# Optimization experiments

Measured on AMD Instinct MI355X. Metric: run time of the kernel, lower is better.

The kernel has to match this reference:

```python
import jax, jax.numpy as jnp
import numpy as np

N, E, D, H, C, HID, ED = 50000, 800000, 128, 8, 16, 512, 32


def setup_inputs() -> dict:
    key = jax.random.key(0)
    ks = jax.random.split(key, 16)
    s = 0.05
    return {
        "h": jax.random.normal(ks[0], (N, D), jnp.float32),
        "edge_index": jax.random.randint(ks[1], (2, E), 0, N, jnp.int64),
        "edge_attr": jax.random.normal(ks[2], (E, ED), jnp.float32),
        "w1": jax.random.normal(ks[3], (D, HID), jnp.float32) * s,
        "b1": jnp.zeros((HID,), jnp.float32),
        "w2": jax.random.normal(ks[4], (HID, D), jnp.float32) * s,
        "b2": jnp.zeros((D,), jnp.float32),
        "ln_g": jnp.ones((D,), jnp.float32),
        "ln_b": jnp.zeros((D,), jnp.float32),
        "Wl": jax.random.normal(ks[5], (D, H * C), jnp.float32) * s,
        "bl": jnp.zeros((H * C,), jnp.float32),
        "Wr": jax.random.normal(ks[6], (D, H * C), jnp.float32) * s,
        "br": jnp.zeros((H * C,), jnp.float32),
        "We": jax.random.normal(ks[7], (ED, H * C), jnp.float32) * s,
        "att": jax.random.normal(ks[8], (H, C), jnp.float32) * s,
        "bias_out": jnp.zeros((H * C,), jnp.float32),
    }


def _layer_norm(x, g, b, eps=1e-5):
    mu = jnp.mean(x, axis=-1, keepdims=True)
    var = jnp.var(x, axis=-1, keepdims=True)
    return (x - mu) * jax.lax.rsqrt(var + eps) * g + b


def reference(h, edge_index, edge_attr, w1, b1, w2, b2, ln_g, ln_b,
              Wl, bl, Wr, br, We, att, bias_out):
    # FFN + residual + LayerNorm (dropout = identity in eval)
    u = jax.nn.relu(h @ w1 + b1) @ w2 + b2
    v = _layer_norm(h + u, ln_g, ln_b)

    src, dst = edge_index[0], edge_index[1]
    # GATv2Conv: separate source/target transforms + edge transform
    xl = (v @ Wl + bl).reshape(N, H, C)
    xr = (v @ Wr + br).reshape(N, H, C)
    xe = (edge_attr @ We).reshape(E, H, C)
    x = jax.nn.leaky_relu(xl[src] + xr[dst] + xe, 0.2)  # [E,H,C]
    logits = jnp.einsum("ehc,hc->eh", x, att)            # [E,H]
    # segment softmax over incoming edges of each destination node
    m = jax.lax.stop_gradient(jax.ops.segment_max(logits, dst, num_segments=N))
    ex = jnp.exp(logits - m[dst])
    den = jax.ops.segment_sum(ex, dst, num_segments=N)
    alpha = ex / den[dst]                                # [E,H]
    msg = xl[src] * alpha[..., None]                     # [E,H,C]
    w = jax.ops.segment_sum(msg, dst, num_segments=N).reshape(N, H * C) + bias_out
    output = _layer_norm(w + v, ln_g, ln_b)
    return output, alpha
```

## Files before the change

kernel.cpp:

```cpp
#include <hip/hip_runtime.h>
#include <math.h>

#define N_NODES 50000
#define E_EDGES 800000
#define D_DIM   128
#define H_HEADS 8
#define C_CH    16
#define HID_DIM 512
#define ED_DIM  32

typedef __attribute__((ext_vector_type(8))) short short8;
typedef __attribute__((ext_vector_type(4))) float f32x4;

__device__ __forceinline__ short f2bf(float f) {
    unsigned u = __float_as_uint(f);
    return (short)((u + 0x7FFFu + ((u >> 16) & 1u)) >> 16);
}
__device__ __forceinline__ float bf2f(short s) {
    return __uint_as_float(((unsigned)(unsigned short)s) << 16);
}

__global__ __launch_bounds__(64) void repack_kernel(
    const float* __restrict__ w1, const float* __restrict__ w2,
    const float* __restrict__ Wl, const float* __restrict__ Wr,
    const float* __restrict__ We,
    short8* __restrict__ w1p, short8* __restrict__ w2p,
    short8* __restrict__ Wlp, short8* __restrict__ Wrp,
    short8* __restrict__ Wep)
{
    int b = blockIdx.x;
    const float* src; short8* dst; int Nw, nc, rel;
    if (b < 128)      { src = w1; dst = w1p; Nw = 512; nc = 4;  rel = b; }
    else if (b < 256) { src = w2; dst = w2p; Nw = 128; nc = 16; rel = b - 128; }
    else if (b < 288) { src = Wl; dst = Wlp; Nw = 128; nc = 4;  rel = b - 256; }
    else if (b < 320) { src = Wr; dst = Wrp; Nw = 128; nc = 4;  rel = b - 288; }
    else              { src = We; dst = Wep; Nw = 128; nc = 1;  rel = b - 320; }
    int t = rel / nc, c = rel % nc;
    int l = threadIdx.x, quad = l >> 4, col = l & 15;
    short8 r;
    #pragma unroll
    for (int j = 0; j < 8; ++j)
        r[j] = f2bf(src[(size_t)(c * 32 + quad * 8 + j) * Nw + t * 16 + col]);
    dst[(size_t)rel * 64 + l] = r;
}

__global__ __launch_bounds__(256) void count_kernel(
    const int* __restrict__ edge_index, unsigned* __restrict__ cnt,
    unsigned short* __restrict__ rank)
{
    int e = blockIdx.x * 256 + threadIdx.x;
    int dst = edge_index[E_EDGES + e];
    rank[e] = (unsigned short)atomicAdd(&cnt[dst], 1u);
}

__global__ __launch_bounds__(256) void node_ffn_mfma(
    const float* __restrict__ h,
    const float* __restrict__ b1, const float* __restrict__ b2,
    const float* __restrict__ ln_g, const float* __restrict__ ln_b,
    const float* __restrict__ bl, const float* __restrict__ br,
    const short8* __restrict__ w1p, const short8* __restrict__ w2p,
    const short8* __restrict__ Wlp, const short8* __restrict__ Wrp,
    float* __restrict__ v_out,
    unsigned short* __restrict__ xl_bf_out, unsigned short* __restrict__ xr_bf_out)
{
    __shared__ short hid_bf[16 * 520];
    __shared__ float v_s[16 * 132];
    __shared__ short v_bf[16 * 136];

    const int tid = threadIdx.x;
    const int w = tid >> 6, lane = tid & 63;
    const int m = lane & 15, quad = lane >> 4;
    const int n0 = blockIdx.x * 16;

    short8 af[4];
    #pragma unroll
    for (int c = 0; c < 4; ++c) {
        const float* hp = h + (size_t)(n0 + m) * 128 + c * 32 + quad * 8;
        float4 p0 = ((const float4*)hp)[0];
        float4 p1 = ((const float4*)hp)[1];
        short8 a;
        a[0] = f2bf(p0.x); a[1] = f2bf(p0.y); a[2] = f2bf(p0.z); a[3] = f2bf(p0.w);
        a[4] = f2bf(p1.x); a[5] = f2bf(p1.y); a[6] = f2bf(p1.z); a[7] = f2bf(p1.w);
        af[c] = a;
    }

    {
        f32x4 acc[8];
        #pragma unroll
        for (int t = 0; t < 8; ++t) acc[t] = (f32x4){0.f, 0.f, 0.f, 0.f};
        #pragma unroll
        for (int t = 0; t < 8; ++t) {
            int tile = w * 8 + t;
            #pragma unroll
            for (int c = 0; c < 4; ++c) {
                short8 bf = w1p[(size_t)(tile * 4 + c) * 64 + lane];
                acc[t] = __builtin_amdgcn_mfma_f32_16x16x32_bf16(af[c], bf, acc[t], 0, 0, 0);
            }
        }
        #pragma unroll
        for (int t = 0; t < 8; ++t) {
            int col = (w * 8 + t) * 16 + m;
            float bias = b1[col];
            #pragma unroll
            for (int r = 0; r < 4; ++r) {
                int row = quad * 4 + r;
                hid_bf[row * 520 + col] = f2bf(fmaxf(acc[t][r] + bias, 0.f));
            }
        }
    }
    __syncthreads();

    {
        f32x4 acc2[2];
        acc2[0] = (f32x4){0.f, 0.f, 0.f, 0.f};
        acc2[1] = (f32x4){0.f, 0.f, 0.f, 0.f};
        #pragma unroll 4
        for (int c = 0; c < 16; ++c) {
            short8 a = *(const short8*)&hid_bf[m * 520 + c * 32 + quad * 8];
            #pragma unroll
            for (int t = 0; t < 2; ++t) {
                short8 bf = w2p[(size_t)((w * 2 + t) * 16 + c) * 64 + lane];
                acc2[t] = __builtin_amdgcn_mfma_f32_16x16x32_bf16(a, bf, acc2[t], 0, 0, 0);
            }
        }
        #pragma unroll
        for (int t = 0; t < 2; ++t) {
            int col = (w * 2 + t) * 16 + m;
            float bias = b2[col];
            #pragma unroll
            for (int r = 0; r < 4; ++r) {
                int row = quad * 4 + r;
                v_s[row * 132 + col] = acc2[t][r] + bias + h[(size_t)(n0 + row) * 128 + col];
            }
        }
    }
    __syncthreads();

    {
        float g0 = ln_g[lane], g1 = ln_g[lane + 64];
        float be0 = ln_b[lane], be1 = ln_b[lane + 64];
        #pragma unroll
        for (int p = 0; p < 4; ++p) {
            int nd = w * 4 + p;
            float x0 = v_s[nd * 132 + lane], x1 = v_s[nd * 132 + lane + 64];
            float s = x0 + x1, ss = x0 * x0 + x1 * x1;
            #pragma unroll
            for (int off = 1; off < 64; off <<= 1) {
                s  += __shfl_xor(s, off);
                ss += __shfl_xor(ss, off);
            }
            float mu = s * (1.f / 128.f);
            float var = ss * (1.f / 128.f) - mu * mu;
            float rs = rsqrtf(var + 1e-5f);
            float y0 = (x0 - mu) * rs * g0 + be0;
            float y1 = (x1 - mu) * rs * g1 + be1;
            v_out[(size_t)(n0 + nd) * 128 + lane]      = y0;
            v_out[(size_t)(n0 + nd) * 128 + lane + 64] = y1;
            v_bf[nd * 136 + lane]      = f2bf(y0);
            v_bf[nd * 136 + lane + 64] = f2bf(y1);
        }
    }
    __syncthreads();

    {
        short8 af3[4];
        #pragma unroll
        for (int c = 0; c < 4; ++c)
            af3[c] = *(const short8*)&v_bf[m * 136 + c * 32 + quad * 8];
        f32x4 accl[2], accr[2];
        #pragma unroll
        for (int t = 0; t < 2; ++t) {
            accl[t] = (f32x4){0.f, 0.f, 0.f, 0.f};
            accr[t] = (f32x4){0.f, 0.f, 0.f, 0.f};
        }
        #pragma unroll
        for (int t = 0; t < 2; ++t) {
            int tile = w * 2 + t;
            #pragma unroll
            for (int c = 0; c < 4; ++c) {
                accl[t] = __builtin_amdgcn_mfma_f32_16x16x32_bf16(
                    af3[c], Wlp[(size_t)(tile * 4 + c) * 64 + lane], accl[t], 0, 0, 0);
                accr[t] = __builtin_amdgcn_mfma_f32_16x16x32_bf16(
                    af3[c], Wrp[(size_t)(tile * 4 + c) * 64 + lane], accr[t], 0, 0, 0);
            }
        }
        #pragma unroll
        for (int t = 0; t < 2; ++t) {
            int col = (w * 2 + t) * 16 + m;
            float bld = bl[col], brd = br[col];
            #pragma unroll
            for (int r = 0; r < 4; ++r) {
                int row = quad * 4 + r;
                xl_bf_out[(size_t)(n0 + row) * 128 + col] = (unsigned short)f2bf(accl[t][r] + bld);
                xr_bf_out[(size_t)(n0 + row) * 128 + col] = (unsigned short)f2bf(accr[t][r] + brd);
            }
        }
    }
}

__global__ __launch_bounds__(1024) void scan_kernel(
    const unsigned* __restrict__ cnt, int* __restrict__ rowstart)
{
    __shared__ int wsum[16];
    __shared__ int s_carry;
    const int t = threadIdx.x, wv = t >> 6, lane = t & 63;
    if (t == 0) s_carry = 0;
    __syncthreads();
    for (int b4 = 0; b4 < N_NODES / 4; b4 += 1024) {
        int i4 = b4 + t;
        int4 v4 = make_int4(0, 0, 0, 0);
        if (i4 < N_NODES / 4) v4 = ((const int4*)cnt)[i4];
        int v = v4.x + v4.y + v4.z + v4.w;
        int s = v;
        #pragma unroll
        for (int off = 1; off < 64; off <<= 1) {
            int nb = __shfl_up(s, off);
            if (lane >= off) s += nb;
        }
        if (lane == 63) wsum[wv] = s;
        __syncthreads();
        int woff = s_carry;
        for (int k = 0; k < wv; ++k) woff += wsum[k];
        int tot = woff + s;
        if (i4 < N_NODES / 4) {
            int e0 = woff + s - v;
            int4 r;
            r.x = e0;
            r.y = e0 + v4.x;
            r.z = r.y + v4.y;
            r.w = r.z + v4.z;
            ((int4*)rowstart)[i4] = r;
        }
        __syncthreads();
        if (t == 1023) s_carry = tot;
    }
}

__global__ __launch_bounds__(256) void scatter_kernel(
    const int* __restrict__ edge_index, const unsigned short* __restrict__ rank,
    const int* __restrict__ rowstart, int* __restrict__ eidx,
    unsigned* __restrict__ srcdst)
{
    int e = blockIdx.x * 256 + threadIdx.x;
    if (e >= E_EDGES) return;
    int src = edge_index[e];
    int dst = edge_index[E_EDGES + e];
    int pos = rowstart[dst] + (int)rank[e];
    eidx[pos] = e;
    srcdst[pos] = (unsigned)src | ((unsigned)dst << 16);
}

__global__ __launch_bounds__(256) void edge_logits_mfma(
    const int* __restrict__ eidx, const unsigned* __restrict__ srcdst,
    const float* __restrict__ edge_attr,
    const short8* __restrict__ Wep, const float* __restrict__ att,
    const unsigned short* __restrict__ xl_bf, const unsigned short* __restrict__ xr_bf,
    float* __restrict__ logits_csr)
{
    __shared__ short8 We_f[512];
    __shared__ short xe_s[64 * 136];
    __shared__ int e_s[64];
    __shared__ unsigned sd_s[64];
    const int tid = threadIdx.x;
    const int w = tid >> 6, lane = tid & 63;
    const int m = lane & 15, quad = lane >> 4;
    const int p0b = blockIdx.x * 64;

    We_f[tid]       = Wep[tid];
    We_f[tid + 256] = Wep[tid + 256];
    if (tid < 64) {
        int pos = p0b + tid;
        e_s[tid]  = eidx[pos];
        sd_s[tid] = srcdst[pos];
    }
    __syncthreads();

    const float* eap = edge_attr + (size_t)e_s[w * 16 + m] * 32 + quad * 8;
    float4 p0 = ((const float4*)eap)[0];
    float4 p1 = ((const float4*)eap)[1];
    short8 a;
    a[0] = f2bf(p0.x); a[1] = f2bf(p0.y); a[2] = f2bf(p0.z); a[3] = f2bf(p0.w);
    a[4] = f2bf(p1.x); a[5] = f2bf(p1.y); a[6] = f2bf(p1.z); a[7] = f2bf(p1.w);

    f32x4 acc[8];
    #pragma unroll
    for (int t = 0; t < 8; ++t) acc[t] = (f32x4){0.f, 0.f, 0.f, 0.f};
    #pragma unroll
    for (int t = 0; t < 8; ++t)
        acc[t] = __builtin_amdgcn_mfma_f32_16x16x32_bf16(a, We_f[t * 64 + lane], acc[t], 0, 0, 0);

    #pragma unroll
    for (int t = 0; t < 8; ++t) {
        #pragma unroll
        for (int r = 0; r < 4; ++r)
            xe_s[(w * 16 + quad * 4 + r) * 136 + t * 16 + m] = f2bf(acc[t][r]);
    }
    __syncthreads();

    const int g = quad;
    const int s = m;
    const int d0 = s * 8;
    float4 at0 = ((const float4*)(att + d0))[0];
    float4 at1 = ((const float4*)(att + d0))[1];

    #pragma unroll
    for (int p = 0; p < 4; ++p) {
        int el = p * 16 + w * 4 + g;
        unsigned sd = sd_s[el];
        int src = (int)(sd & 0xffffu);
        int dst = (int)(sd >> 16);
        short8 xl8 = *(const short8*)&xl_bf[(size_t)src * 128 + d0];
        short8 xr8 = *(const short8*)&xr_bf[(size_t)dst * 128 + d0];
        short8 xe8 = *(const short8*)&xe_s[el * 136 + d0];

        float atv[8] = { at0.x, at0.y, at0.z, at0.w, at1.x, at1.y, at1.z, at1.w };
        float pq = 0.f;
        #pragma unroll
        for (int dd = 0; dd < 8; ++dd) {
            float x = bf2f(xl8[dd]) + bf2f(xr8[dd]) + bf2f(xe8[dd]);
            x = (x > 0.f) ? x : 0.2f * x;
            pq += x * atv[dd];
        }
        pq += __shfl_xor(pq, 1);
        if ((s & 1) == 0)
            logits_csr[(size_t)(p0b + el) * 8 + (s >> 1)] = pq;
    }
}

__global__ __launch_bounds__(256) void node_aggregate_kernel(
    const int* __restrict__ eidx, const int* __restrict__ rowstart,
    const unsigned* __restrict__ cnt, const unsigned* __restrict__ srcdst,
    const float* __restrict__ logits_csr,
    const unsigned short* __restrict__ xl_bf, const float* __restrict__ v,
    const float* __restrict__ bias_out,
    const float* __restrict__ ln_g, const float* __restrict__ ln_b,
    float* __restrict__ alpha_out, float* __restrict__ out)
{
    const int wv = threadIdx.x >> 6, lane = threadIdx.x & 63;
    const int n = blockIdx.x * 4 + wv;
    if (n >= N_NODES) return;
    const int start = rowstart[n];
    const int num = (int)cnt[n];

    const int hh = lane & 7;
    const int slot = lane >> 3;

    float den = 0.f;
    for (int i = slot; i < num; i += 8) {
        den += expf(logits_csr[(size_t)(start + i) * 8 + hh]);
    }
    den += __shfl_xor(den, 8);
    den += __shfl_xor(den, 16);
    den += __shfl_xor(den, 32);
    float inv = 1.f / den;

    const int g = lane >> 4, s = lane & 15;
    const int h3 = s >> 1;
    float iv3 = __shfl(inv, h3);
    float acc[8] = {0.f, 0.f, 0.f, 0.f, 0.f, 0.f, 0.f, 0.f};
    for (int i = 0; i < num; i += 4) {
        int ii = i + g;
        if (ii < num) {
            int e = eidx[start + ii];
            int src = (int)(srcdst[start + ii] & 0xffffu);
            float lg = logits_csr[(size_t)(start + ii) * 8 + h3];
            float al = expf(lg) * iv3;
            if ((s & 1) == 0) alpha_out[(size_t)e * 8 + h3] = al;
            short8 q = *(const short8*)&xl_bf[(size_t)src * 128 + s * 8];
            acc[0] += bf2f(q[0]) * al; acc[1] += bf2f(q[1]) * al;
            acc[2] += bf2f(q[2]) * al; acc[3] += bf2f(q[3]) * al;
            acc[4] += bf2f(q[4]) * al; acc[5] += bf2f(q[5]) * al;
            acc[6] += bf2f(q[6]) * al; acc[7] += bf2f(q[7]) * al;
        }
    }
    #pragma unroll
    for (int k = 0; k < 8; ++k) {
        acc[k] += __shfl_xor(acc[k], 16);
        acc[k] += __shfl_xor(acc[k], 32);
    }

    const float* vp = v + (size_t)n * 128 + s * 8;
    float4 v0 = ((const float4*)vp)[0], v1 = ((const float4*)vp)[1];
    float4 b0 = ((const float4*)(bias_out + s * 8))[0];
    float4 b1 = ((const float4*)(bias_out + s * 8))[1];
    float x[8];
    x[0] = acc[0] + b0.x + v0.x; x[1] = acc[1] + b0.y + v0.y;
    x[2] = acc[2] + b0.z + v0.z; x[3] = acc[3] + b0.w + v0.w;
    x[4] = acc[4] + b1.x + v1.x; x[5] = acc[5] + b1.y + v1.y;
    x[6] = acc[6] + b1.z + v1.z; x[7] = acc[7] + b1.w + v1.w;
    float sm = 0.f, ssm = 0.f;
    #pragma unroll
    for (int k = 0; k < 8; ++k) { sm += x[k]; ssm += x[k] * x[k]; }
    #pragma unroll
    for (int off = 1; off < 16; off <<= 1) {
        sm  += __shfl_xor(sm, off);
        ssm += __shfl_xor(ssm, off);
    }
    float mu = sm * (1.f / 128.f);
    float var = ssm * (1.f / 128.f) - mu * mu;
    float rs = rsqrtf(var + 1e-5f);
    if (g == 0) {
        float4 g0 = ((const float4*)(ln_g + s * 8))[0];
        float4 g1 = ((const float4*)(ln_g + s * 8))[1];
        float4 be0 = ((const float4*)(ln_b + s * 8))[0];
        float4 be1 = ((const float4*)(ln_b + s * 8))[1];
        float4 o0, o1;
        o0.x = (x[0] - mu) * rs * g0.x + be0.x;
        o0.y = (x[1] - mu) * rs * g0.y + be0.y;
        o0.z = (x[2] - mu) * rs * g0.z + be0.z;
        o0.w = (x[3] - mu) * rs * g0.w + be0.w;
        o1.x = (x[4] - mu) * rs * g1.x + be1.x;
        o1.y = (x[5] - mu) * rs * g1.y + be1.y;
        o1.z = (x[6] - mu) * rs * g1.z + be1.z;
        o1.w = (x[7] - mu) * rs * g1.w + be1.w;
        float4* op = (float4*)(out + (size_t)n * 128 + s * 8);
        op[0] = o0; op[1] = o1;
    }
}

extern "C" void kernel_launch(void* const* d_in, const int* in_sizes, int n_in,
                              void* d_out, int out_size, void* d_ws, size_t ws_size,
                              hipStream_t stream)
{
    const float* h        = (const float*)d_in[0];
    const int*   edge_idx = (const int*)  d_in[1];
    const float* edge_attr= (const float*)d_in[2];
    const float* w1       = (const float*)d_in[3];
    const float* b1       = (const float*)d_in[4];
    const float* w2       = (const float*)d_in[5];
    const float* b2       = (const float*)d_in[6];
    const float* ln_g     = (const float*)d_in[7];
    const float* ln_b     = (const float*)d_in[8];
    const float* Wl       = (const float*)d_in[9];
    const float* bl       = (const float*)d_in[10];
    const float* Wr       = (const float*)d_in[11];
    const float* br       = (const float*)d_in[12];
    const float* We       = (const float*)d_in[13];
    const float* att      = (const float*)d_in[14];
    const float* bias_out = (const float*)d_in[15];

    float* out   = (float*)d_out;
    float* alpha = out + (size_t)N_NODES * 128;

    short8* w1p = (short8*)alpha;
    short8* w2p = w1p + 128 * 64;
    short8* Wlp = w2p + 128 * 64;
    short8* Wrp = Wlp + 32 * 64;

    float*          v        = (float*)d_ws;
    unsigned short* xl_bf    = (unsigned short*)(v + (size_t)N_NODES*128);
    unsigned short* xr_bf    = xl_bf + (size_t)N_NODES * 128;
    float*          lcsr     = (float*)(xr_bf + (size_t)N_NODES * 128);
    unsigned*       cnt      = (unsigned*)(lcsr + (size_t)E_EDGES * 8);
    int*            rowstart = (int*)(cnt + N_NODES);
    unsigned short* rank     = (unsigned short*)(rowstart + N_NODES);
    short8*         Wep      = (short8*)(rank + E_EDGES);
    int*            eidx     = (int*)(Wep + 512);
    unsigned*       srcdst   = (unsigned*)(eidx + E_EDGES);

    hipMemsetAsync(cnt, 0, (size_t)N_NODES * sizeof(unsigned), stream);

    repack_kernel<<<328, 64, 0, stream>>>(w1, w2, Wl, Wr, We,
                                          w1p, w2p, Wlp, Wrp, Wep);
    count_kernel<<<E_EDGES / 256, 256, 0, stream>>>(edge_idx, cnt, rank);
    node_ffn_mfma<<<N_NODES / 16, 256, 0, stream>>>(
        h, b1, b2, ln_g, ln_b, bl, br, w1p, w2p, Wlp, Wrp, v, xl_bf, xr_bf);
    scan_kernel<<<1, 1024, 0, stream>>>(cnt, rowstart);
    scatter_kernel<<<(E_EDGES + 255) / 256, 256, 0, stream>>>(
        edge_idx, rank, rowstart, eidx, srcdst);
    edge_logits_mfma<<<E_EDGES / 64, 256, 0, stream>>>(
        eidx, srcdst, edge_attr, Wep, att, xl_bf, xr_bf, lcsr);
    node_aggregate_kernel<<<(N_NODES + 3) / 4, 256, 0, stream>>>(
        eidx, rowstart, cnt, srcdst, lcsr, xl_bf, v, bias_out, ln_g, ln_b, alpha, out);
}
```

Baseline: 452.8 us.

## Fold softmax denominator into single aggregation pass with deferred normalization

The edge kernel now stores exp(logit) instead of the raw logit, and the aggregation kernel accumulates both the unnormalized weighted message and the per-head denominator in one pass over incoming edges. It then scales by 1/den at the end, and alpha is written in a separate tail loop. This drops the separate denominator pass and one of the two exp evaluations per edge. Like the code before, it skips the max subtraction, so a large logit could overflow exp. Alpha is written in a second read of exbuf, with the store layout now indexed by head per lane.

```diff
diff --git a/kernel.cpp b/kernel.cpp
--- a/kernel.cpp
+++ b/kernel.cpp
@@ -255,7 +255,7 @@
     const float* __restrict__ edge_attr,
     const short8* __restrict__ Wep, const float* __restrict__ att,
     const unsigned short* __restrict__ xl_bf, const unsigned short* __restrict__ xr_bf,
-    float* __restrict__ logits_csr)
+    float* __restrict__ exbuf)
 {
     __shared__ short8 We_f[512];
     __shared__ short xe_s[64 * 136];
@@ -323,14 +323,14 @@
         }
         pq += __shfl_xor(pq, 1);
         if ((s & 1) == 0)
-            logits_csr[(size_t)(p0b + el) * 8 + (s >> 1)] = pq;
+            exbuf[(size_t)(p0b + el) * 8 + (s >> 1)] = expf(pq);
     }
 }
 
 __global__ __launch_bounds__(256) void node_aggregate_kernel(
     const int* __restrict__ eidx, const int* __restrict__ rowstart,
     const unsigned* __restrict__ cnt, const unsigned* __restrict__ srcdst,
-    const float* __restrict__ logits_csr,
+    const float* __restrict__ exbuf,
     const unsigned short* __restrict__ xl_bf, const float* __restrict__ v,
     const float* __restrict__ bias_out,
     const float* __restrict__ ln_g, const float* __restrict__ ln_b,
@@ -342,35 +342,22 @@
     const int start = rowstart[n];
     const int num = (int)cnt[n];
 
-    const int hh = lane & 7;
-    const int slot = lane >> 3;
-
-    float den = 0.f;
-    for (int i = slot; i < num; i += 8) {
-        den += expf(logits_csr[(size_t)(start + i) * 8 + hh]);
-    }
-    den += __shfl_xor(den, 8);
-    den += __shfl_xor(den, 16);
-    den += __shfl_xor(den, 32);
-    float inv = 1.f / den;
-
     const int g = lane >> 4, s = lane & 15;
     const int h3 = s >> 1;
-    float iv3 = __shfl(inv, h3);
     float acc[8] = {0.f, 0.f, 0.f, 0.f, 0.f, 0.f, 0.f, 0.f};
+    float den = 0.f;
     for (int i = 0; i < num; i += 4) {
         int ii = i + g;
         if (ii < num) {
-            int e = eidx[start + ii];
-            int src = (int)(srcdst[start + ii] & 0xffffu);
-            float lg = logits_csr[(size_t)(start + ii) * 8 + h3];
-            float al = expf(lg) * iv3;
-            if ((s & 1) == 0) alpha_out[(size_t)e * 8 + h3] = al;
+            int pos = start + ii;
+            int src = (int)(srcdst[pos] & 0xffffu);
+            float ex = exbuf[(size_t)pos * 8 + h3];
+            if ((s & 1) == 0) den += ex;
             short8 q = *(const short8*)&xl_bf[(size_t)src * 128 + s * 8];
-            acc[0] += bf2f(q[0]) * al; acc[1] += bf2f(q[1]) * al;
-            acc[2] += bf2f(q[2]) * al; acc[3] += bf2f(q[3]) * al;
-            acc[4] += bf2f(q[4]) * al; acc[5] += bf2f(q[5]) * al;
-            acc[6] += bf2f(q[6]) * al; acc[7] += bf2f(q[7]) * al;
+            acc[0] += bf2f(q[0]) * ex; acc[1] += bf2f(q[1]) * ex;
+            acc[2] += bf2f(q[2]) * ex; acc[3] += bf2f(q[3]) * ex;
+            acc[4] += bf2f(q[4]) * ex; acc[5] += bf2f(q[5]) * ex;
+            acc[6] += bf2f(q[6]) * ex; acc[7] += bf2f(q[7]) * ex;
         }
     }
     #pragma unroll
@@ -378,16 +365,20 @@
         acc[k] += __shfl_xor(acc[k], 16);
         acc[k] += __shfl_xor(acc[k], 32);
     }
+    den += __shfl_xor(den, 16);
+    den += __shfl_xor(den, 32);
+    float den_h = __shfl(den, 2 * h3);
+    float inv = (num > 0) ? (1.f / den_h) : 0.f;
 
     const float* vp = v + (size_t)n * 128 + s * 8;
     float4 v0 = ((const float4*)vp)[0], v1 = ((const float4*)vp)[1];
     float4 b0 = ((const float4*)(bias_out + s * 8))[0];
     float4 b1 = ((const float4*)(bias_out + s * 8))[1];
     float x[8];
-    x[0] = acc[0] + b0.x + v0.x; x[1] = acc[1] + b0.y + v0.y;
-    x[2] = acc[2] + b0.z + v0.z; x[3] = acc[3] + b0.w + v0.w;
-    x[4] = acc[4] + b1.x + v1.x; x[5] = acc[5] + b1.y + v1.y;
-    x[6] = acc[6] + b1.z + v1.z; x[7] = acc[7] + b1.w + v1.w;
+    x[0] = acc[0] * inv + b0.x + v0.x; x[1] = acc[1] * inv + b0.y + v0.y;
+    x[2] = acc[2] * inv + b0.z + v0.z; x[3] = acc[3] * inv + b0.w + v0.w;
+    x[4] = acc[4] * inv + b1.x + v1.x; x[5] = acc[5] * inv + b1.y + v1.y;
+    x[6] = acc[6] * inv + b1.z + v1.z; x[7] = acc[7] * inv + b1.w + v1.w;
     float sm = 0.f, ssm = 0.f;
     #pragma unroll
     for (int k = 0; k < 8; ++k) { sm += x[k]; ssm += x[k] * x[k]; }
@@ -416,6 +407,17 @@
         float4* op = (float4*)(out + (size_t)n * 128 + s * 8);
         op[0] = o0; op[1] = o1;
     }
+
+    if (num > 0) {
+        const int h7 = lane & 7, j8 = lane >> 3;
+        float invh = __shfl(inv, 2 * h7);
+        for (int i = j8; i < num; i += 8) {
+            int pos = start + i;
+            float ex = exbuf[(size_t)pos * 8 + h7];
+            int e = eidx[pos];
+            alpha_out[(size_t)e * 8 + h7] = ex * invh;
+        }
+    }
 }
 
 extern "C" void kernel_launch(void* const* d_in, const int* in_sizes, int n_in,
@@ -450,8 +452,8 @@
     float*          v        = (float*)d_ws;
     unsigned short* xl_bf    = (unsigned short*)(v + (size_t)N_NODES*128);
     unsigned short* xr_bf    = xl_bf + (size_t)N_NODES * 128;
-    float*          lcsr     = (float*)(xr_bf + (size_t)N_NODES * 128);
-    unsigned*       cnt      = (unsigned*)(lcsr + (size_t)E_EDGES * 8);
+    float*          exbuf    = (float*)(xr_bf + (size_t)N_NODES * 128);
+    unsigned*       cnt      = (unsigned*)(exbuf + (size_t)E_EDGES * 8);
     int*            rowstart = (int*)(cnt + N_NODES);
     unsigned short* rank     = (unsigned short*)(rowstart + N_NODES);
     short8*         Wep      = (short8*)(rank + E_EDGES);
@@ -469,7 +471,7 @@
     scatter_kernel<<<(E_EDGES + 255) / 256, 256, 0, stream>>>(
         edge_idx, rank, rowstart, eidx, srcdst);
     edge_logits_mfma<<<E_EDGES / 64, 256, 0, stream>>>(
-        eidx, srcdst, edge_attr, Wep, att, xl_bf, xr_bf, lcsr);
+        eidx, srcdst, edge_attr, Wep, att, xl_bf, xr_bf, exbuf);
     node_aggregate_kernel<<<(N_NODES + 3) / 4, 256, 0, stream>>>(
-        eidx, rowstart, cnt, srcdst, lcsr, xl_bf, v, bias_out, ln_g, ln_b, alpha, out);
-}
+        eidx, rowstart, cnt, srcdst, exbuf, xl_bf, v, bias_out, ln_g, ln_b, alpha, out);
+}
```

Result: faster. 442.2 us (-2.3%).
